# Kernel tuning notes

Measured on AMD Instinct MI355X. Metric: run time of the kernel, lower is better.

The kernel has to match this reference:

```python
import jax, jax.numpy as jnp
import numpy as np

WS = 8          # window_size
HEADS = 8
DIM_HEAD = 32
SCALE = DIM_HEAD ** -0.5

# relative position indices (ws^2, ws^2, 2), offset by ws-1 -> in [0, 2*ws-2]
_idx = np.array([[i, j] for i in range(WS) for j in range(WS)])
_rel = _idx[None, :, :] - _idx[:, None, :] + (WS - 1)
REL_I = jnp.asarray(_rel[..., 0])
REL_J = jnp.asarray(_rel[..., 1])


def setup_inputs() -> dict:
    key = jax.random.key(0)
    k0, k1, k2, k3 = jax.random.split(key, 4)
    dim = HEADS * DIM_HEAD  # 256
    x = jax.random.normal(k0, (2, 4, 128, 128, dim), dtype=jnp.float32)
    w_qkv = jax.random.normal(k1, (3 * dim, dim), dtype=jnp.float32) * 0.02
    pos_embedding = jax.random.normal(k2, (2 * WS - 1, 2 * WS - 1), dtype=jnp.float32)
    w_out = jax.random.normal(k3, (dim, dim), dtype=jnp.float32) * 0.02
    b_out = jnp.zeros((dim,), dtype=jnp.float32)
    return {"x": x, "w_qkv": w_qkv, "pos_embedding": pos_embedding,
            "w_out": w_out, "b_out": b_out}


def _to_windows(t, b, l, nh, nw):
    # (b,l,H,W,m*c) -> (b,l,m,nh*nw,ws*ws,c)
    t = t.reshape(b, l, nh, WS, nw, WS, HEADS, DIM_HEAD)
    t = t.transpose(0, 1, 6, 2, 4, 3, 5, 7)
    return t.reshape(b, l, HEADS, nh * nw, WS * WS, DIM_HEAD)


def reference(x, w_qkv, pos_embedding, w_out, b_out):
    b, l, H, W, c = x.shape
    nh, nw = H // WS, W // WS
    qkv = jnp.einsum('blhwc,oc->blhwo', x, w_qkv)  # to_qkv, no bias
    q, k, v = jnp.split(qkv, 3, axis=-1)
    q = _to_windows(q, b, l, nh, nw)
    k = _to_windows(k, b, l, nh, nw)
    v = _to_windows(v, b, l, nh, nw)
    dots = jnp.einsum('blmhic,blmhjc->blmhij', q, k) * SCALE
    dots = dots + pos_embedding[REL_I, REL_J]  # gathered relative-pos bias
    attn = jax.nn.softmax(dots, axis=-1)
    out = jnp.einsum('blmhij,blmhjc->blmhic', attn, v)
    # (b,l,m,nh*nw,ws*ws,c) -> (b,l,H,W,m*c)
    out = out.reshape(b, l, HEADS, nh, nw, WS, WS, DIM_HEAD)
    out = out.transpose(0, 1, 3, 5, 4, 6, 2, 7).reshape(b, l, H, W, HEADS * DIM_HEAD)
    return jnp.einsum('blhwc,oc->blhwo', out, w_out) + b_out
```

## Files before the change

### kernel.cpp

```cpp
#include <hip/hip_runtime.h>


typedef __attribute__((ext_vector_type(8))) short bf16x8;
typedef __attribute__((ext_vector_type(4))) float f32x4;

#define MFMA16(a,b,c) __builtin_amdgcn_mfma_f32_16x16x32_bf16(a,b,c,0,0,0)
#define SCALE 0.17677669529663687f
#define WS_QKV_BYTES 393216
#define WS_TOTAL_BYTES 524288
#define PEG_OFF 65536

__device__ __forceinline__ short bfr(float f) {
    unsigned u = __builtin_bit_cast(unsigned, f);
    u = (u + 0x7FFFu + ((u >> 16) & 1u)) >> 16;
    return (short)u;
}
__device__ __forceinline__ unsigned pkbf(float lo, float hi) {
    unsigned r;
    asm("v_cvt_pk_bf16_f32 %0, %1, %2" : "=v"(r) : "v"(lo), "v"(hi));
    return r;
}

__device__ __forceinline__ bf16x8 cvt8(const float* gp) {
    float4 f0 = *reinterpret_cast<const float4*>(gp);
    float4 f1 = *reinterpret_cast<const float4*>(gp + 4);
    float fv[8] = {f0.x,f0.y,f0.z,f0.w,f1.x,f1.y,f1.z,f1.w};
    bf16x8 r;
    #pragma unroll
    for (int j = 0; j < 8; ++j) r[j] = bfr(fv[j]);
    return r;
}

__global__ void prep_kernel(const float* __restrict__ wqkv, const float* __restrict__ wout,
                            char* __restrict__ ws) {
    int t = blockIdx.x * 256 + threadIdx.x;
    const float* src;
    int byt;
    if (t < 24576) {
        int o = t >> 5, kc = t & 31;
        src = wqkv + o * 256 + kc * 8;
        byt = ((o >> 4) * 8 + (kc >> 2)) * 1024 + ((kc & 3) * 16 + (o & 15)) * 16;
    } else {
        int t2 = t - 24576;
        int o = t2 >> 5, kc = t2 & 31;
        src = wout + o * 256 + kc * 8;
        byt = WS_QKV_BYTES + ((o >> 4) * 8 + (kc >> 2)) * 1024 + ((kc & 3) * 16 + (o & 15)) * 16;
    }
    *reinterpret_cast<bf16x8*>(ws + byt) = cvt8(src);
}

template<bool USE_WS>
__global__ __launch_bounds__(512, 4)
void winattn_kernel(const float* __restrict__ x, const float* __restrict__ wqkv,
                    const float* __restrict__ peg, const float* __restrict__ wout,
                    const float* __restrict__ bout, float* __restrict__ out,
                    const char* __restrict__ wsb)
{
    __shared__ __align__(16) char lds[66560];
    const int tid = threadIdx.x;
    const int wave = tid >> 6, lane = tid & 63;
    const int lg = lane >> 4, ln = lane & 15;
    const int img = blockIdx.x >> 8, win = blockIdx.x & 255;
    const size_t base = ((size_t)(img * 128 + (win >> 4) * 8) * 128 + (win & 15) * 8) * 256;
    const int lswz = (ln & 7) << 4;

    #pragma unroll
    for (int i = 0; i < 4; ++i) {
        int ch = tid + i * 512;
        int t = ch >> 5, cc = ch & 31;
        const float* gp = x + base + (size_t)(((t >> 3) * 128 + (t & 7)) * 256 + cc * 8);
        float4 f0 = *reinterpret_cast<const float4*>(gp);
        float4 f1 = *reinterpret_cast<const float4*>(gp + 4);
        int4 w;
        w.x = (int)pkbf(f0.x, f0.y); w.y = (int)pkbf(f0.z, f0.w);
        w.z = (int)pkbf(f1.x, f1.y); w.w = (int)pkbf(f1.z, f1.w);
        *reinterpret_cast<int4*>(lds + ((t * 512 + cc * 16) ^ ((t & 7) << 4))) = w;
    }
    if (tid < 225) ((float*)(lds + PEG_OFF))[tid] = peg[tid];
    __syncthreads();

    f32x4 aqk[4][4];
    f32x4 av[4][2];
    #pragma unroll
    for (int a = 0; a < 4; ++a) {
        #pragma unroll
        for (int b = 0; b < 4; ++b) aqk[a][b] = (f32x4){0.f,0.f,0.f,0.f};
        #pragma unroll
        for (int b = 0; b < 2; ++b) av[a][b] = (f32x4){0.f,0.f,0.f,0.f};
    }
    const int fl = (lg * 16 + ln) * 16;
    #pragma unroll 1
    for (int kk = 0; kk < 8; ++kk) {
        bf16x8 ah[4];
        #pragma unroll
        for (int mt = 0; mt < 4; ++mt)
            ah[mt] = *reinterpret_cast<const bf16x8*>(
                lds + (((mt * 16 + ln) * 512 + kk * 64 + lg * 16) ^ lswz));
        #pragma unroll
        for (int nv = 0; nv < 6; ++nv) {
            bf16x8 bh;
            if constexpr (USE_WS) {
                bh = *reinterpret_cast<const bf16x8*>(
                    wsb + (((nv >> 1) * 16 + wave * 2 + (nv & 1)) * 8 + kk) * 1024 + fl);
            } else {
                int o = (nv >> 1) * 256 + wave * 32 + (nv & 1) * 16 + ln;
                bh = cvt8(wqkv + (size_t)o * 256 + kk * 32 + lg * 8);
            }
            if (nv < 4) {
                #pragma unroll
                for (int mt = 0; mt < 4; ++mt)
                    aqk[mt][nv] = MFMA16(bh, ah[mt], aqk[mt][nv]);
            } else {
                #pragma unroll
                for (int mt = 0; mt < 4; ++mt)
                    av[mt][nv - 4] = MFMA16(ah[mt], bh, av[mt][nv - 4]);
            }
        }
    }
    __syncthreads();

    char* slc = lds + wave * 8192;

    #pragma unroll
    for (int mt = 0; mt < 4; ++mt)
        #pragma unroll
        for (int u = 0; u < 2; ++u) {
            int lin = (mt * 16 + ln) * 64 + u * 32 + lg * 8;
            uint2 wq = make_uint2(pkbf(aqk[mt][u][0], aqk[mt][u][1]),
                                  pkbf(aqk[mt][u][2], aqk[mt][u][3]));
            uint2 wk = make_uint2(pkbf(aqk[mt][2 + u][0], aqk[mt][2 + u][1]),
                                  pkbf(aqk[mt][2 + u][2], aqk[mt][2 + u][3]));
            *reinterpret_cast<uint2*>(slc + (lin ^ lswz)) = wq;
            *reinterpret_cast<uint2*>(slc + 4096 + (lin ^ lswz)) = wk;
        }
    bf16x8 aq[4], bk[4];
    #pragma unroll
    for (int mi = 0; mi < 4; ++mi) {
        int lin = ((mi * 16 + ln) * 64 + lg * 16) ^ lswz;
        aq[mi] = *reinterpret_cast<const bf16x8*>(slc + lin);
        bk[mi] = *reinterpret_cast<const bf16x8*>(slc + 4096 + lin);
    }

    #pragma unroll
    for (int mt = 0; mt < 4; ++mt)
        #pragma unroll
        for (int u = 0; u < 2; ++u) {
            int d = u * 16 + ln;
            int lin = d * 128 + mt * 32 + lg * 8;
            uint2 w = make_uint2(pkbf(av[mt][u][0], av[mt][u][1]),
                                 pkbf(av[mt][u][2], av[mt][u][3]));
            *reinterpret_cast<uint2*>(slc + (lin ^ lswz)) = w;
        }

    f32x4 sc[4][4];
    #pragma unroll
    for (int mi = 0; mi < 4; ++mi)
        #pragma unroll
        for (int nj = 0; nj < 4; ++nj)
            sc[mi][nj] = MFMA16(bk[nj], aq[mi], ((f32x4){0.f,0.f,0.f,0.f}));

    const char* bp = lds + PEG_OFF - 360 +
        4 * ((((lg >> 1) - (ln >> 3) + 7) * 15) + (lg & 1) * 4 - (ln & 7) + 7);

    float pinv[4];
    bf16x8 ap[4][2];
    #pragma unroll
    for (int mi = 0; mi < 4; ++mi) {
        #pragma unroll
        for (int nj = 0; nj < 4; ++nj)
            #pragma unroll
            for (int r = 0; r < 4; ++r)
                sc[mi][nj][r] = fmaf(sc[mi][nj][r], SCALE,
                    *reinterpret_cast<const float*>(bp + 360 + 120 * (nj - mi) + 4 * r));
        float mx = sc[mi][0][0];
        #pragma unroll
        for (int nj = 0; nj < 4; ++nj)
            #pragma unroll
            for (int r = 0; r < 4; ++r) mx = fmaxf(mx, sc[mi][nj][r]);
        mx = fmaxf(mx, __shfl_xor(mx, 16));
        mx = fmaxf(mx, __shfl_xor(mx, 32));
        float sum = 0.f;
        #pragma unroll
        for (int nj = 0; nj < 4; ++nj)
            #pragma unroll
            for (int r = 0; r < 4; ++r) {
                float e = __expf(sc[mi][nj][r] - mx);
                sc[mi][nj][r] = e;
                sum += e;
            }
        sum += __shfl_xor(sum, 16);
        sum += __shfl_xor(sum, 32);
        pinv[mi] = 1.f / sum;
        #pragma unroll
        for (int kkv = 0; kkv < 2; ++kkv) {
            int4 t;
            t.x = (int)pkbf(sc[mi][2 * kkv][0],     sc[mi][2 * kkv][1]);
            t.y = (int)pkbf(sc[mi][2 * kkv][2],     sc[mi][2 * kkv][3]);
            t.z = (int)pkbf(sc[mi][2 * kkv + 1][0], sc[mi][2 * kkv + 1][1]);
            t.w = (int)pkbf(sc[mi][2 * kkv + 1][2], sc[mi][2 * kkv + 1][3]);
            ap[mi][kkv] = __builtin_bit_cast(bf16x8, t);
        }
    }

    f32x4 po[2][4];
    #pragma unroll
    for (int u = 0; u < 2; ++u)
        #pragma unroll
        for (int mi = 0; mi < 4; ++mi) po[u][mi] = (f32x4){0.f,0.f,0.f,0.f};
    #pragma unroll
    for (int kkv = 0; kkv < 2; ++kkv) {
        bf16x8 bvf[2];
        #pragma unroll
        for (int u = 0; u < 2; ++u) {
            int d = u * 16 + ln;
            int lin0 = d * 128 + kkv * 64 + lg * 8;
            uint2 lo = *reinterpret_cast<const uint2*>(slc + (lin0 ^ lswz));
            uint2 hi = *reinterpret_cast<const uint2*>(slc + ((lin0 + 32) ^ lswz));
            int4 t; t.x = (int)lo.x; t.y = (int)lo.y; t.z = (int)hi.x; t.w = (int)hi.y;
            bvf[u] = __builtin_bit_cast(bf16x8, t);
        }
        #pragma unroll
        for (int u = 0; u < 2; ++u)
            #pragma unroll
            for (int mi = 0; mi < 4; ++mi)
                po[u][mi] = MFMA16(bvf[u], ap[mi][kkv], po[u][mi]);
    }

    #pragma unroll
    for (int u = 0; u < 2; ++u)
        #pragma unroll
        for (int mi = 0; mi < 4; ++mi) {
            int lin = (mi * 16 + ln) * 64 + u * 32 + lg * 8;
            uint2 w = make_uint2(pkbf(po[u][mi][0] * pinv[mi], po[u][mi][1] * pinv[mi]),
                                 pkbf(po[u][mi][2] * pinv[mi], po[u][mi][3] * pinv[mi]));
            *reinterpret_cast<uint2*>(slc + 4096 + (lin ^ lswz)) = w;
        }
    __syncthreads();

    f32x4 fo[4][2];
    #pragma unroll
    for (int mi = 0; mi < 4; ++mi)
        #pragma unroll
        for (int u = 0; u < 2; ++u) fo[mi][u] = (f32x4){0.f,0.f,0.f,0.f};
    float bo0 = bout[wave * 32 + ln];
    float bo1 = bout[wave * 32 + 16 + ln];

    #pragma unroll 1
    for (int hh = 0; hh < 8; ++hh) {
        const char* ahh = lds + hh * 8192 + 4096;
        bf16x8 aa[4];
        #pragma unroll
        for (int mi = 0; mi < 4; ++mi)
            aa[mi] = *reinterpret_cast<const bf16x8*>(ahh + ((((mi * 16 + ln) * 64) + lg * 16) ^ lswz));
        bf16x8 bb[2];
        #pragma unroll
        for (int u = 0; u < 2; ++u) {
            if constexpr (USE_WS) {
                bb[u] = *reinterpret_cast<const bf16x8*>(
                    wsb + WS_QKV_BYTES + ((wave * 2 + u) * 8 + hh) * 1024 + fl);
            } else {
                int oc = wave * 32 + u * 16 + ln;
                bb[u] = cvt8(wout + (size_t)oc * 256 + hh * 32 + lg * 8);
            }
        }
        #pragma unroll
        for (int mi = 0; mi < 4; ++mi)
            #pragma unroll
            for (int u = 0; u < 2; ++u)
                fo[mi][u] = MFMA16(aa[mi], bb[u], fo[mi][u]);
    }

    #pragma unroll
    for (int mi = 0; mi < 4; ++mi)
        #pragma unroll
        for (int r = 0; r < 4; ++r) {
            int t = mi * 16 + lg * 4 + r;
            float* op = out + base + (size_t)(((t >> 3) * 128 + (t & 7)) * 256);
            op[wave * 32 + ln]      = fo[mi][0][r] + bo0;
            op[wave * 32 + 16 + ln] = fo[mi][1][r] + bo1;
        }
}

extern "C" void kernel_launch(void* const* d_in, const int* in_sizes, int n_in,
                              void* d_out, int out_size, void* d_ws, size_t ws_size,
                              hipStream_t stream) {
    const float* x    = (const float*)d_in[0];
    const float* wqkv = (const float*)d_in[1];
    const float* peg  = (const float*)d_in[2];
    const float* wout = (const float*)d_in[3];
    const float* bout = (const float*)d_in[4];
    float* out = (float*)d_out;
    if (d_ws != nullptr && ws_size >= WS_TOTAL_BYTES) {
        hipLaunchKernelGGL(prep_kernel, dim3(128), dim3(256), 0, stream,
                           wqkv, wout, (char*)d_ws);
        hipLaunchKernelGGL((winattn_kernel<true>), dim3(2048), dim3(512), 0, stream,
                           x, wqkv, peg, wout, bout, out, (const char*)d_ws);
    } else {
        hipLaunchKernelGGL((winattn_kernel<false>), dim3(2048), dim3(512), 0, stream,
                           x, wqkv, peg, wout, bout, out, nullptr);
    }
}
```

Measured before the change: 125.7 us.

## Fold softmax scale into Wq, bias into MFMA accumulator, drop max, vectorize output

Pre-scales the Q weights by scale*log2(e) so the attention scores come out of the MFMA already scaled. The relative-position bias, also multiplied by log2(e), is preloaded as the MFMA accumulator init, and exp2 replaces expf. The max-subtraction pass and its cross-lane shuffles are removed, which risks overflow if scores get large. The output projection swaps its MFMA operands so each lane holds 4 contiguous output channels, starts the accumulator from the bias, and writes float4 stores instead of scalar stores.

```diff
diff --git a/kernel.cpp b/kernel.cpp
--- a/kernel.cpp
+++ b/kernel.cpp
@@ -6,6 +6,8 @@
 
 #define MFMA16(a,b,c) __builtin_amdgcn_mfma_f32_16x16x32_bf16(a,b,c,0,0,0)
 #define SCALE 0.17677669529663687f
+#define L2E   1.4426950408889634f
+#define QSC   (SCALE * L2E)
 #define WS_QKV_BYTES 393216
 #define WS_TOTAL_BYTES 524288
 #define PEG_OFF 65536
@@ -21,13 +23,13 @@
     return r;
 }
 
-__device__ __forceinline__ bf16x8 cvt8(const float* gp) {
+__device__ __forceinline__ bf16x8 cvt8s(const float* gp, float s) {
     float4 f0 = *reinterpret_cast<const float4*>(gp);
     float4 f1 = *reinterpret_cast<const float4*>(gp + 4);
     float fv[8] = {f0.x,f0.y,f0.z,f0.w,f1.x,f1.y,f1.z,f1.w};
     bf16x8 r;
     #pragma unroll
-    for (int j = 0; j < 8; ++j) r[j] = bfr(fv[j]);
+    for (int j = 0; j < 8; ++j) r[j] = bfr(fv[j] * s);
     return r;
 }
 
@@ -36,17 +38,19 @@
     int t = blockIdx.x * 256 + threadIdx.x;
     const float* src;
     int byt;
+    float s = 1.f;
     if (t < 24576) {
         int o = t >> 5, kc = t & 31;
         src = wqkv + o * 256 + kc * 8;
         byt = ((o >> 4) * 8 + (kc >> 2)) * 1024 + ((kc & 3) * 16 + (o & 15)) * 16;
+        if (o < 256) s = QSC;
     } else {
         int t2 = t - 24576;
         int o = t2 >> 5, kc = t2 & 31;
         src = wout + o * 256 + kc * 8;
         byt = WS_QKV_BYTES + ((o >> 4) * 8 + (kc >> 2)) * 1024 + ((kc & 3) * 16 + (o & 15)) * 16;
     }
-    *reinterpret_cast<bf16x8*>(ws + byt) = cvt8(src);
+    *reinterpret_cast<bf16x8*>(ws + byt) = cvt8s(src, s);
 }
 
 template<bool USE_WS>
@@ -104,7 +108,7 @@
                     wsb + (((nv >> 1) * 16 + wave * 2 + (nv & 1)) * 8 + kk) * 1024 + fl);
             } else {
                 int o = (nv >> 1) * 256 + wave * 32 + (nv & 1) * 16 + ln;
-                bh = cvt8(wqkv + (size_t)o * 256 + kk * 32 + lg * 8);
+                bh = cvt8s(wqkv + (size_t)o * 256 + kk * 32 + lg * 8, nv < 2 ? QSC : 1.f);
             }
             if (nv < 4) {
                 #pragma unroll
@@ -141,6 +145,15 @@
         bk[mi] = *reinterpret_cast<const bf16x8*>(slc + 4096 + lin);
     }
 
+    const char* bp = lds + PEG_OFF - 360 +
+        4 * ((((lg >> 1) - (ln >> 3) + 7) * 15) + (lg & 1) * 4 - (ln & 7) + 7);
+    f32x4 bC[7];
+    #pragma unroll
+    for (int d = 0; d < 7; ++d)
+        #pragma unroll
+        for (int r = 0; r < 4; ++r)
+            bC[d][r] = L2E * *reinterpret_cast<const float*>(bp + 120 * d + 4 * r);
+
     #pragma unroll
     for (int mt = 0; mt < 4; ++mt)
         #pragma unroll
@@ -157,34 +170,18 @@
     for (int mi = 0; mi < 4; ++mi)
         #pragma unroll
         for (int nj = 0; nj < 4; ++nj)
-            sc[mi][nj] = MFMA16(bk[nj], aq[mi], ((f32x4){0.f,0.f,0.f,0.f}));
-
-    const char* bp = lds + PEG_OFF - 360 +
-        4 * ((((lg >> 1) - (ln >> 3) + 7) * 15) + (lg & 1) * 4 - (ln & 7) + 7);
+            sc[mi][nj] = MFMA16(bk[nj], aq[mi], bC[nj - mi + 3]);
 
     float pinv[4];
     bf16x8 ap[4][2];
     #pragma unroll
     for (int mi = 0; mi < 4; ++mi) {
-        #pragma unroll
-        for (int nj = 0; nj < 4; ++nj)
-            #pragma unroll
-            for (int r = 0; r < 4; ++r)
-                sc[mi][nj][r] = fmaf(sc[mi][nj][r], SCALE,
-                    *reinterpret_cast<const float*>(bp + 360 + 120 * (nj - mi) + 4 * r));
-        float mx = sc[mi][0][0];
-        #pragma unroll
-        for (int nj = 0; nj < 4; ++nj)
-            #pragma unroll
-            for (int r = 0; r < 4; ++r) mx = fmaxf(mx, sc[mi][nj][r]);
-        mx = fmaxf(mx, __shfl_xor(mx, 16));
-        mx = fmaxf(mx, __shfl_xor(mx, 32));
         float sum = 0.f;
         #pragma unroll
         for (int nj = 0; nj < 4; ++nj)
             #pragma unroll
             for (int r = 0; r < 4; ++r) {
-                float e = __expf(sc[mi][nj][r] - mx);
+                float e = __builtin_amdgcn_exp2f(sc[mi][nj][r]);
                 sc[mi][nj][r] = e;
                 sum += e;
             }
@@ -237,13 +234,14 @@
         }
     __syncthreads();
 
+    float4 fi0 = *reinterpret_cast<const float4*>(bout + wave * 32 + lg * 4);
+    float4 fi1 = *reinterpret_cast<const float4*>(bout + wave * 32 + 16 + lg * 4);
     f32x4 fo[4][2];
     #pragma unroll
-    for (int mi = 0; mi < 4; ++mi)
-        #pragma unroll
-        for (int u = 0; u < 2; ++u) fo[mi][u] = (f32x4){0.f,0.f,0.f,0.f};
-    float bo0 = bout[wave * 32 + ln];
-    float bo1 = bout[wave * 32 + 16 + ln];
+    for (int mi = 0; mi < 4; ++mi) {
+        fo[mi][0] = (f32x4){fi0.x, fi0.y, fi0.z, fi0.w};
+        fo[mi][1] = (f32x4){fi1.x, fi1.y, fi1.z, fi1.w};
+    }
 
     #pragma unroll 1
     for (int hh = 0; hh < 8; ++hh) {
@@ -260,25 +258,23 @@
                     wsb + WS_QKV_BYTES + ((wave * 2 + u) * 8 + hh) * 1024 + fl);
             } else {
                 int oc = wave * 32 + u * 16 + ln;
-                bb[u] = cvt8(wout + (size_t)oc * 256 + hh * 32 + lg * 8);
+                bb[u] = cvt8s(wout + (size_t)oc * 256 + hh * 32 + lg * 8, 1.f);
             }
         }
         #pragma unroll
         for (int mi = 0; mi < 4; ++mi)
             #pragma unroll
             for (int u = 0; u < 2; ++u)
-                fo[mi][u] = MFMA16(aa[mi], bb[u], fo[mi][u]);
-    }
-
-    #pragma unroll
-    for (int mi = 0; mi < 4; ++mi)
-        #pragma unroll
-        for (int r = 0; r < 4; ++r) {
-            int t = mi * 16 + lg * 4 + r;
-            float* op = out + base + (size_t)(((t >> 3) * 128 + (t & 7)) * 256);
-            op[wave * 32 + ln]      = fo[mi][0][r] + bo0;
-            op[wave * 32 + 16 + ln] = fo[mi][1][r] + bo1;
-        }
+                fo[mi][u] = MFMA16(bb[u], aa[mi], fo[mi][u]);
+    }
+
+    #pragma unroll
+    for (int mi = 0; mi < 4; ++mi) {
+        int t = mi * 16 + ln;
+        float* op = out + base + (size_t)(((t >> 3) * 128 + (t & 7)) * 256 + wave * 32 + lg * 4);
+        *reinterpret_cast<float4*>(op)      = *reinterpret_cast<float4*>(&fo[mi][0]);
+        *reinterpret_cast<float4*>(op + 16) = *reinterpret_cast<float4*>(&fo[mi][1]);
+    }
 }
 
 extern "C" void kernel_launch(void* const* d_in, const int* in_sizes, int n_in,
```

Result: slower. 136.4 us (+8.6%).
